# Kernel optimization log

Measured on AMD Instinct MI355X. Metric: run time of the kernel, lower is better.

The kernel has to match this reference:

```python
import jax, jax.numpy as jnp
import numpy as np

NODES = 81
NODE_DIM = 2
IN_DIM = NODES * NODE_DIM  # 162
D = 256
H = 16
HD = D // H
DFF = 2048
T, B, E = 1024, 8, 648


def _layernorm(x, w, b, eps=1e-5):
    m = x.mean(-1, keepdims=True)
    v = x.var(-1, keepdims=True)
    return (x - m) / jnp.sqrt(v + eps) * w + b


def setup_inputs() -> dict:
    key = jax.random.key(0)
    ks = jax.random.split(key, 12)
    s = 0.02
    W = lambda k, shape: jax.random.normal(k, shape, jnp.float32) * s
    return {
        "src": jax.random.normal(ks[0], (T, B, IN_DIM), jnp.float32),
        "edge_index": jax.random.randint(ks[1], (2, E), 0, NODES),
        "gcn_w": W(ks[2], (NODE_DIM, NODE_DIM)),
        "gcn_b": jnp.zeros((NODE_DIM,), jnp.float32),
        "fc_w": W(ks[3], (IN_DIM, D)),
        "fc_b": jnp.zeros((D,), jnp.float32),
        "wq": W(ks[4], (D, D)), "bq": jnp.zeros((D,), jnp.float32),
        "wk": W(ks[5], (D, D)), "bk": jnp.zeros((D,), jnp.float32),
        "wv": W(ks[6], (D, D)), "bv": jnp.zeros((D,), jnp.float32),
        "wo": W(ks[7], (D, D)), "bo": jnp.zeros((D,), jnp.float32),
        "ln1_w": jnp.ones((D,), jnp.float32), "ln1_b": jnp.zeros((D,), jnp.float32),
        "ffn_w1": W(ks[8], (D, DFF)), "ffn_b1": jnp.zeros((DFF,), jnp.float32),
        "ffn_w2": W(ks[9], (DFF, D)), "ffn_b2": jnp.zeros((D,), jnp.float32),
        "ln2_w": jnp.ones((D,), jnp.float32), "ln2_b": jnp.zeros((D,), jnp.float32),
        "dec_w": W(ks[10], (D, IN_DIM)), "dec_b": jnp.zeros((IN_DIM,), jnp.float32),
    }


def reference(src, edge_index, gcn_w, gcn_b, fc_w, fc_b, wq, bq, wk, bk, wv, bv,
              wo, bo, ln1_w, ln1_b, ffn_w1, ffn_b1, ffn_w2, ffn_b2, ln2_w, ln2_b,
              dec_w, dec_b):
    t, b, _ = src.shape
    # ---- batched GCNConv(2,2): all T*B tiny graphs share one adjacency ----
    # src[t,b] = [in_flow(81), out_flow(81)] -> node features [81, 2]
    xg = jnp.swapaxes(src.reshape(t, b, NODE_DIM, NODES), -1, -2)  # [T,B,81,2]
    row, col = edge_index[0], edge_index[1]
    A = jnp.zeros((NODES, NODES), src.dtype).at[col, row].add(1.0)
    A = A + jnp.eye(NODES, dtype=src.dtype)          # add self-loops
    deg = A.sum(1)
    dinv = jnp.where(deg > 0, 1.0 / jnp.sqrt(deg), 0.0)
    A_hat = dinv[:, None] * A * dinv[None, :]        # D^-1/2 (A+I) D^-1/2
    hg = jnp.einsum('ij,tbjc->tbic', A_hat, xg @ gcn_w) + gcn_b  # [T,B,81,2]
    # gcn_output.transpose(0,1).view(-1): channel-major flatten
    src2 = jnp.swapaxes(hg, -1, -2).reshape(t, b, IN_DIM)
    # ---- fc + positional encoding ----
    x = src2 @ fc_w + fc_b  # [T,B,D]
    pos = jnp.arange(t, dtype=jnp.float32)[:, None]
    div = jnp.exp(jnp.arange(0, D, 2, dtype=jnp.float32) * (-np.log(10000.0) / D))
    pe = jnp.zeros((t, D), x.dtype).at[:, 0::2].set(jnp.sin(pos * div))
    pe = pe.at[:, 1::2].set(jnp.cos(pos * div))
    x = x + pe[:, None, :]
    # ---- TransformerEncoderLayer (post-norm, relu, causal mask, eval) ----
    q = (x @ wq + bq).reshape(t, b, H, HD)
    k = (x @ wk + bk).reshape(t, b, H, HD)
    v = (x @ wv + bv).reshape(t, b, H, HD)
    scores = jnp.einsum('tbhd,sbhd->bhts', q, k) / jnp.sqrt(jnp.asarray(HD, x.dtype))
    causal = jnp.tril(jnp.ones((t, t), bool))
    scores = jnp.where(causal, scores, jnp.finfo(x.dtype).min)
    attn = jax.nn.softmax(scores, axis=-1)
    ctx = jnp.einsum('bhts,sbhd->tbhd', attn, v).reshape(t, b, D) @ wo + bo
    x = _layernorm(x + ctx, ln1_w, ln1_b)
    ff = jax.nn.relu(x @ ffn_w1 + ffn_b1) @ ffn_w2 + ffn_b2
    x = _layernorm(x + ff, ln2_w, ln2_b)
    return x @ dec_w + dec_b  # [T,B,162]
```

## Files before the change

### kernel.cpp

```cpp
#include <hip/hip_runtime.h>
#include <math.h>

#define T_    1024
#define B_    8
#define D_    256
#define H_    16
#define HD_   16
#define DFF_  2048
#define NODES_ 81
#define INDIM_ 162
#define E_    648
#define M_    (T_*B_)

typedef __bf16 bf16x8 __attribute__((ext_vector_type(8)));
typedef float  f32x4  __attribute__((ext_vector_type(4)));
typedef unsigned short ushort_t;
typedef unsigned int   uint_t;

union bfpack { bf16x8 v; uint_t u[4]; };

__device__ __forceinline__ ushort_t f2bf(float f) {
    union { float f; uint_t u; } c; c.f = f;
    uint_t u = c.u;
    uint_t r = u + 0x7fffu + ((u >> 16) & 1u);
    return (ushort_t)(r >> 16);
}

__device__ __forceinline__ uint_t fbits(float f) {
    union { float f; uint_t u; } c; c.f = f;
    return c.u;
}

__device__ __forceinline__ float truncbf(float f) {
    union { uint_t u; float f; } c; c.u = fbits(f) & 0xffff0000u;
    return c.f;
}

__device__ __forceinline__ bf16x8 zero8() {
    bf16x8 v;
#pragma unroll
    for (int e = 0; e < 8; e++) v[e] = (__bf16)0.0f;
    return v;
}

__device__ __forceinline__ void gload_lds16(const void* g, void* l) {
    __builtin_amdgcn_global_load_lds(
        (const __attribute__((address_space(1))) void*)g,
        (__attribute__((address_space(3))) void*)l, 16, 0, 0);
}

__device__ __forceinline__ void trans_tile(
        const float* __restrict__ in, ushort_t* __restrict__ out,
        float (*tile)[33], int K, int N, int Kp, int bx, int by) {
    int k0 = bx * 32, n0 = by * 32;
    int tx = threadIdx.x & 31, ty = threadIdx.x >> 5;
#pragma unroll
    for (int i = 0; i < 4; i++) {
        int r = k0 + ty + i * 8, c = n0 + tx;
        tile[ty + i * 8][tx] = (r < K && c < N) ? in[(size_t)r * N + c] : 0.f;
    }
    __syncthreads();
#pragma unroll
    for (int i = 0; i < 4; i++) {
        int r = n0 + ty + i * 8, c = k0 + tx;
        out[(size_t)r * Kp + c] = f2bf(tile[tx][ty + i * 8]);
    }
}

__global__ __launch_bounds__(256) void prep_all(
        const int* __restrict__ edge, const float* __restrict__ gcn_w,
        const float* __restrict__ gcn_b, const float* __restrict__ fc_w,
        const float* __restrict__ fc_b, const float* __restrict__ src,
        const float* __restrict__ wq, const float* __restrict__ wk,
        const float* __restrict__ wv, const float* __restrict__ wo,
        const float* __restrict__ dec_w, const float* __restrict__ w1,
        const float* __restrict__ w2,
        const float* __restrict__ bq, const float* __restrict__ bk,
        const float* __restrict__ bv,
        ushort_t* __restrict__ weffT, float* __restrict__ beff,
        ushort_t* __restrict__ srcb,
        ushort_t* __restrict__ wqkvT, ushort_t* __restrict__ woT,
        ushort_t* __restrict__ dwT, ushort_t* __restrict__ w1T,
        ushort_t* __restrict__ w2T, float* __restrict__ qkvbias) {
    __shared__ float A[NODES_ * NODES_];
    __shared__ float dinv[NODES_];
    __shared__ float tile[32][33];
    int bid = blockIdx.x;
    int tid = threadIdx.x;
    if (bid < 82) {
        for (int i = tid; i < NODES_ * NODES_; i += 256) A[i] = 0.f;
        __syncthreads();
        for (int e = tid; e < E_; e += 256) {
            int r = edge[e];
            int c = edge[E_ + e];
            atomicAdd(&A[c * NODES_ + r], 1.0f);
        }
        __syncthreads();
        if (tid < NODES_) A[tid * NODES_ + tid] += 1.0f;
        __syncthreads();
        if (tid < NODES_) {
            float s = 0.f;
            for (int k = 0; k < NODES_; k++) s += A[tid * NODES_ + k];
            dinv[tid] = (s > 0.f) ? rsqrtf(s) : 0.f;
        }
        __syncthreads();
        int d = tid, j = bid;
        if (j < NODES_) {
            float s0 = 0.f, s1 = 0.f;
            for (int i = 0; i < NODES_; i++) {
                float a = dinv[i] * A[i * NODES_ + j] * dinv[j];
                s0 += a * fc_w[(0 * NODES_ + i) * D_ + d];
                s1 += a * fc_w[(1 * NODES_ + i) * D_ + d];
            }
            weffT[d * 192 + j]          = f2bf(gcn_w[0] * s0 + gcn_w[1] * s1);
            weffT[d * 192 + NODES_ + j] = f2bf(gcn_w[2] * s0 + gcn_w[3] * s1);
        } else {
            float t0 = 0.f, t1 = 0.f;
            for (int i = 0; i < NODES_; i++) {
                t0 += fc_w[(0 * NODES_ + i) * D_ + d];
                t1 += fc_w[(1 * NODES_ + i) * D_ + d];
            }
            beff[d] = fc_b[d] + gcn_b[0] * t0 + gcn_b[1] * t1;
            for (int c = INDIM_; c < 192; c++) weffT[d * 192 + c] = 0;
        }
    } else if (bid < 1426) {
        int l = bid - 82;
        if (l < 64)        trans_tile(wq,    wqkvT,          tile, D_,   D_,     D_,   l & 7,  l >> 3);
        else if (l < 128)  trans_tile(wk,    wqkvT + 65536,  tile, D_,   D_,     D_,   (l-64) & 7,  (l-64) >> 3);
        else if (l < 192)  trans_tile(wv,    wqkvT + 131072, tile, D_,   D_,     D_,   (l-128) & 7, (l-128) >> 3);
        else if (l < 256)  trans_tile(wo,    woT,            tile, D_,   D_,     D_,   (l-192) & 7, (l-192) >> 3);
        else if (l < 320)  trans_tile(dec_w, dwT,            tile, D_,   INDIM_, D_,   (l-256) & 7, (l-256) >> 3);
        else if (l < 832)  trans_tile(w1,    w1T,            tile, D_,   DFF_,   D_,   (l-320) & 7, (l-320) >> 3);
        else               trans_tile(w2,    w2T,            tile, DFF_, D_,     DFF_, (l-832) & 63, (l-832) >> 6);
    } else if (bid == 1426) {
#pragma unroll
        for (int k = 0; k < 3; k++) {
            int i = k * 256 + tid;
            qkvbias[i] = (i < 256) ? bq[i] : ((i < 512) ? bk[i - 256] : bv[i - 512]);
        }
    } else {
        int r = bid - 1427;
        if (tid < 192)
            srcb[(size_t)r * 192 + tid] =
                (tid < INDIM_) ? f2bf(src[(size_t)r * INDIM_ + tid]) : (ushort_t)0;
    }
}

enum { EP_PE = 0, EP_QKV = 1, EP_PLAIN = 2, EP_RELU = 3, EP_DEC = 4, EP_PART = 5 };

template <int EPI, int TM, int KS>
__global__ __launch_bounds__(256) void gemm_bf16(
        const ushort_t* __restrict__ A, const ushort_t* __restrict__ BT,
        const float* __restrict__ bias, float* __restrict__ Cf,
        ushort_t* __restrict__ Cb, int M, int N, int K) {
    __shared__ ushort_t sA[TM * 64];
    __shared__ ushort_t sB[128 * 64];
    int tid = threadIdx.x;
    int w = tid >> 6, lane = tid & 63;
    int cc = lane & 15, q = lane >> 4;
    int bm = blockIdx.y * TM, bn = blockIdx.x * 128;
    int part = (KS > 1) ? blockIdx.z : 0;
    int kbeg = part * (K / KS), kend = kbeg + K / KS;

    int srow = (lane >> 3);
    int sslot = lane & 7;

    const int NJ = (TM == 128) ? 4 : 2;
    int mbase = (TM == 128) ? ((w >> 1) * 64) : 0;
    int nbase = (TM == 128) ? ((w & 1) * 64) : (w * 32);

    f32x4 acc[4][NJ];
#pragma unroll
    for (int i = 0; i < 4; i++)
#pragma unroll
        for (int j = 0; j < NJ; j++)
#pragma unroll
            for (int e = 0; e < 4; e++) acc[i][j][e] = 0.f;

    for (int k0 = kbeg; k0 < kend; k0 += 64) {
        if (TM == 128) {
#pragma unroll
            for (int i = 0; i < 4; i++) {
                int r = w * 32 + i * 8 + srow;
                const ushort_t* ga = A + (size_t)(bm + r) * K + k0 + ((sslot ^ (r & 7)) * 8);
                gload_lds16(ga, &sA[(w * 32 + i * 8) * 64]);
            }
        } else {
#pragma unroll
            for (int i = 0; i < 2; i++) {
                int r = w * 16 + i * 8 + srow;
                const ushort_t* ga = A + (size_t)(bm + r) * K + k0 + ((sslot ^ (r & 7)) * 8);
                gload_lds16(ga, &sA[(w * 16 + i * 8) * 64]);
            }
        }
#pragma unroll
        for (int i = 0; i < 4; i++) {
            int r = w * 32 + i * 8 + srow;
            const ushort_t* gb = BT + (size_t)(bn + r) * K + k0 + ((sslot ^ (r & 7)) * 8);
            gload_lds16(gb, &sB[(w * 32 + i * 8) * 64]);
        }
        __syncthreads();
#pragma unroll
        for (int ks = 0; ks < 2; ks++) {
            bf16x8 af[4], bfr[NJ];
#pragma unroll
            for (int i = 0; i < 4; i++) {
                int m = mbase + i * 16 + cc;
                int off = m * 64 + (((ks * 4 + q) ^ (cc & 7)) * 8);
                af[i] = *(const bf16x8*)&sA[off];
            }
#pragma unroll
            for (int j = 0; j < NJ; j++) {
                int n = nbase + j * 16 + cc;
                int off = n * 64 + (((ks * 4 + q) ^ (cc & 7)) * 8);
                bfr[j] = *(const bf16x8*)&sB[off];
            }
#pragma unroll
            for (int i = 0; i < 4; i++)
#pragma unroll
                for (int j = 0; j < NJ; j++)
                    acc[i][j] = __builtin_amdgcn_mfma_f32_16x16x32_bf16(af[i], bfr[j], acc[i][j], 0, 0, 0);
        }
        __syncthreads();
    }

#pragma unroll
    for (int i = 0; i < 4; i++) {
#pragma unroll
        for (int j = 0; j < NJ; j++) {
            int col = bn + nbase + j * 16 + cc;
            float bv = 0.f;
            if (EPI == EP_DEC) bv = (col < INDIM_) ? bias[col] : 0.f;
            else if (EPI != EP_PART) bv = bias[col];
#pragma unroll
            for (int reg = 0; reg < 4; reg++) {
                int row = bm + mbase + i * 16 + q * 4 + reg;
                float v = acc[i][j][reg] + bv;
                if (EPI == EP_PE) {
                    int t = row >> 3;
                    float freq = __expf((float)(col & ~1) * (-9.210340371976184f / 256.f));
                    float ang = (float)t * freq;
                    v += (col & 1) ? __cosf(ang) : __sinf(ang);
                    Cf[(size_t)row * N + col] = v;
                    Cb[(size_t)row * N + col] = f2bf(v);
                } else if (EPI == EP_QKV) {
                    int t = row >> 3, b = row & 7;
                    int nn = col & 255, which = col >> 8;
                    int h = nn >> 4, hd = nn & 15;
                    Cb[(size_t)which * 2097152 +
                       ((size_t)((b * H_ + h) * T_ + t)) * HD_ + hd] = f2bf(v);
                } else if (EPI == EP_PLAIN) {
                    Cf[(size_t)row * N + col] = v;
                } else if (EPI == EP_RELU) {
                    v = fmaxf(v, 0.f);
                    Cb[(size_t)row * N + col] = f2bf(v);
                } else if (EPI == EP_DEC) {
                    if (col < INDIM_) Cf[(size_t)row * INDIM_ + col] = v;
                } else if (EPI == EP_PART) {
                    Cf[(size_t)part * M * N + (size_t)row * N + col] = v;
                }
            }
        }
    }
}

__global__ __launch_bounds__(256) void attn_mfma(
        const ushort_t* __restrict__ Qb, const ushort_t* __restrict__ Kb,
        const ushort_t* __restrict__ Vb, float* __restrict__ partO,
        float* __restrict__ partL) {
    const int qc_of[20] = {0,1,2,2,3,3,4,4,4,5,5,5,6,6,6,6,7,7,7,7};
    const int kp_of[20] = {0,0,0,1,0,1,0,1,2,0,1,2,0,1,2,3,0,1,2,3};
    int slot = blockIdx.x;
    int qc = qc_of[slot], kp = kp_of[slot];
    int bh = blockIdx.y;
    int tid = threadIdx.x;
    int w = tid >> 6, lane = tid & 63;
    int cc = lane & 15, q = lane >> 4;
    int qb0 = qc * 128;
    int kbeg = kp * 4;
    int kend = 2 * (qc + 1);
    if (kend > kbeg + 4) kend = kbeg + 4;

    __shared__ ushort_t VTs[2][16 * 72];

    const ushort_t* Qp = Qb + (size_t)bh * (T_ * HD_);
    const ushort_t* Kp = Kb + (size_t)bh * (T_ * HD_);
    const ushort_t* Vp = Vb + (size_t)bh * (T_ * HD_);

    bf16x8 qf[2];
#pragma unroll
    for (int i = 0; i < 2; i++) {
        if (q < 2)
            qf[i] = *(const bf16x8*)&Qp[(size_t)(qb0 + w * 32 + i * 16 + cc) * HD_ + q * 8];
        else
            qf[i] = zero8();
    }

    f32x4 ot[2];
    float lacc[2] = {0.f, 0.f};
#pragma unroll
    for (int i = 0; i < 2; i++)
#pragma unroll
        for (int e = 0; e < 4; e++) ot[i][e] = 0.f;

    int qmaxw = qb0 + w * 32 + 31;

    for (int kb = kbeg; kb < kend; kb++) {
        ushort_t* vbuf = VTs[kb & 1];
        if (tid < 128) {
            int r = tid >> 1, half = tid & 1;
            bf16x8 vv = *(const bf16x8*)&Vp[(size_t)(kb * 64 + r) * HD_ + half * 8];
#pragma unroll
            for (int e = 0; e < 8; e++)
                vbuf[(half * 8 + e) * 72 + r] = ((const ushort_t*)&vv)[e];
        }
        __syncthreads();
        if (kb * 64 > qmaxw) continue;

        f32x4 s[2][4];
#pragma unroll
        for (int j = 0; j < 4; j++) {
            bf16x8 kf;
            if (q < 2)
                kf = *(const bf16x8*)&Kp[(size_t)(kb * 64 + j * 16 + cc) * HD_ + q * 8];
            else
                kf = zero8();
#pragma unroll
            for (int i = 0; i < 2; i++) {
                f32x4 z;
#pragma unroll
                for (int e = 0; e < 4; e++) z[e] = 0.f;
                s[i][j] = __builtin_amdgcn_mfma_f32_16x16x32_bf16(kf, qf[i], z, 0, 0, 0);
            }
        }

#pragma unroll
        for (int j = 0; j < 4; j++) {
            bfpack af;
            const uint_t* vt = (const uint_t*)&vbuf[cc * 72 + j * 16 + q * 4];
            af.u[0] = vt[0]; af.u[1] = vt[1]; af.u[2] = 0u; af.u[3] = 0u;
            int key0 = kb * 64 + j * 16 + q * 4;
#pragma unroll
            for (int i = 0; i < 2; i++) {
                int qrow = qb0 + w * 32 + i * 16 + cc;
                float p0 = __expf(s[i][j][0] * 0.25f);
                float p1 = __expf(s[i][j][1] * 0.25f);
                float p2 = __expf(s[i][j][2] * 0.25f);
                float p3 = __expf(s[i][j][3] * 0.25f);
                if (key0 + 0 > qrow) p0 = 0.f;
                if (key0 + 1 > qrow) p1 = 0.f;
                if (key0 + 2 > qrow) p2 = 0.f;
                if (key0 + 3 > qrow) p3 = 0.f;
                bfpack pf;
                pf.u[0] = (fbits(p0) >> 16) | (fbits(p1) & 0xffff0000u);
                pf.u[1] = (fbits(p2) >> 16) | (fbits(p3) & 0xffff0000u);
                pf.u[2] = 0u; pf.u[3] = 0u;
                ot[i] = __builtin_amdgcn_mfma_f32_16x16x32_bf16(af.v, pf.v, ot[i], 0, 0, 0);
                lacc[i] += truncbf(p0) + truncbf(p1) + truncbf(p2) + truncbf(p3);
            }
        }
    }

    int base = (bh * 20 + slot) * 128;
#pragma unroll
    for (int i = 0; i < 2; i++) {
        float l0 = lacc[i];
        l0 += __shfl_xor(l0, 16);
        l0 += __shfl_xor(l0, 32);
        int row = w * 32 + i * 16 + cc;
        *(f32x4*)&partO[((size_t)(base + row)) * 16 + q * 4] = ot[i];
        if (q == 0) partL[base + row] = l0;
    }
}

__global__ __launch_bounds__(256) void attn_reduce(
        const float* __restrict__ partO, const float* __restrict__ partL,
        ushort_t* __restrict__ ctxb) {
    const int cum[9] = {0, 1, 2, 4, 6, 9, 12, 16, 20};
    int qc = blockIdx.x, bh = blockIdx.y;
    int row = threadIdx.x >> 1, dh = threadIdx.x & 1;
    int p0 = cum[qc], p1 = cum[qc + 1];
    float o[8];
#pragma unroll
    for (int e = 0; e < 8; e++) o[e] = 0.f;
    float l = 0.f;
    for (int p = p0; p < p1; p++) {
        size_t base = ((size_t)bh * 20 + p) * 128 + row;
        const float4 a = *(const float4*)&partO[base * 16 + dh * 8];
        const float4 b4 = *(const float4*)&partO[base * 16 + dh * 8 + 4];
        o[0] += a.x; o[1] += a.y; o[2] += a.z; o[3] += a.w;
        o[4] += b4.x; o[5] += b4.y; o[6] += b4.z; o[7] += b4.w;
        l += partL[base];
    }
    float inv = 1.f / l;
    int t = qc * 128 + row, b = bh >> 4, h = bh & 15;
    ushort_t* op = ctxb + ((size_t)t * B_ + b) * D_ + h * HD_ + dh * 8;
    ushort4 u0, u1;
    u0.x = f2bf(o[0] * inv); u0.y = f2bf(o[1] * inv);
    u0.z = f2bf(o[2] * inv); u0.w = f2bf(o[3] * inv);
    u1.x = f2bf(o[4] * inv); u1.y = f2bf(o[5] * inv);
    u1.z = f2bf(o[6] * inv); u1.w = f2bf(o[7] * inv);
    *(ushort4*)&op[0] = u0;
    *(ushort4*)&op[4] = u1;
}

template <int NP, bool HASB>
__global__ __launch_bounds__(256) void ln_kernel(
        const float* __restrict__ X, const float* __restrict__ P0,
        const float* __restrict__ P1, const float* __restrict__ RB,
        const float* __restrict__ w, const float* __restrict__ b,
        float* __restrict__ out, ushort_t* __restrict__ outb) {
    int wv = threadIdx.x >> 6, lane = threadIdx.x & 63;
    int row = blockIdx.x * 4 + wv;
    int c = lane * 4;
    const float4 x4 = *(const float4*)&X[(size_t)row * D_ + c];
    const float4 p4 = *(const float4*)&P0[(size_t)row * D_ + c];
    float v0 = x4.x + p4.x, v1 = x4.y + p4.y, v2 = x4.z + p4.z, v3 = x4.w + p4.w;
    if (NP == 2) {
        const float4 q4 = *(const float4*)&P1[(size_t)row * D_ + c];
        v0 += q4.x; v1 += q4.y; v2 += q4.z; v3 += q4.w;
    }
    if (HASB) {
        const float4 r4 = *(const float4*)&RB[c];
        v0 += r4.x; v1 += r4.y; v2 += r4.z; v3 += r4.w;
    }
    float s  = v0 + v1 + v2 + v3;
    float sq = v0 * v0 + v1 * v1 + v2 * v2 + v3 * v3;
    for (int off = 32; off; off >>= 1) {
        s  += __shfl_xor(s, off);
        sq += __shfl_xor(sq, off);
    }
    float mean = s * (1.f / 256.f);
    float var  = sq * (1.f / 256.f) - mean * mean;
    float rstd = rsqrtf(var + 1e-5f);
    float o0 = (v0 - mean) * rstd * w[c + 0] + b[c + 0];
    float o1 = (v1 - mean) * rstd * w[c + 1] + b[c + 1];
    float o2 = (v2 - mean) * rstd * w[c + 2] + b[c + 2];
    float o3 = (v3 - mean) * rstd * w[c + 3] + b[c + 3];
    float4 o; o.x = o0; o.y = o1; o.z = o2; o.w = o3;
    *(float4*)&out[(size_t)row * D_ + c] = o;
    ushort4 ob;
    ob.x = f2bf(o0); ob.y = f2bf(o1); ob.z = f2bf(o2); ob.w = f2bf(o3);
    *(ushort4*)&outb[(size_t)row * D_ + c] = ob;
}

extern "C" void kernel_launch(void* const* d_in, const int* in_sizes, int n_in,
                              void* d_out, int out_size, void* d_ws, size_t ws_size,
                              hipStream_t stream) {
    (void)in_sizes; (void)n_in; (void)out_size; (void)ws_size;
    const float* src     = (const float*)d_in[0];
    const int*   edge    = (const int*)d_in[1];
    const float* gcn_w   = (const float*)d_in[2];
    const float* gcn_b   = (const float*)d_in[3];
    const float* fc_w    = (const float*)d_in[4];
    const float* fc_b    = (const float*)d_in[5];
    const float* wq      = (const float*)d_in[6];
    const float* bq      = (const float*)d_in[7];
    const float* wk      = (const float*)d_in[8];
    const float* bk      = (const float*)d_in[9];
    const float* wv      = (const float*)d_in[10];
    const float* bv      = (const float*)d_in[11];
    const float* wo      = (const float*)d_in[12];
    const float* bo      = (const float*)d_in[13];
    const float* ln1_w   = (const float*)d_in[14];
    const float* ln1_b   = (const float*)d_in[15];
    const float* ffn_w1  = (const float*)d_in[16];
    const float* ffn_b1  = (const float*)d_in[17];
    const float* ffn_w2  = (const float*)d_in[18];
    const float* ffn_b2  = (const float*)d_in[19];
    const float* ln2_w   = (const float*)d_in[20];
    const float* ln2_b   = (const float*)d_in[21];
    const float* dec_w   = (const float*)d_in[22];
    const float* dec_b   = (const float*)d_in[23];
    float* out = (float*)d_out;

    float* ws = (float*)d_ws;
    float* beff    = ws;
    float* qkvbias = ws + 256;
    float* x0      = ws + 1024;
    float* tmp     = x0  + 2097152;
    float* tmp2    = tmp + 2097152;
    float* x1      = tmp2 + 2097152;
    float* x2s     = x1  + 2097152;
    ushort_t* ub   = (ushort_t*)(ws + 10486784);
    ushort_t* srcb = ub;
    ushort_t* x0b  = ub + 1572864;
    ushort_t* x1b  = x0b + 2097152;
    ushort_t* x2b  = x1b + 2097152;
    ushort_t* ctxb = x2b + 2097152;
    ushort_t* hb   = ctxb + 2097152;
    ushort_t* qkvb = hb + 16777216;
    ushort_t* weffT= qkvb + 6291456;
    ushort_t* wqkvT= weffT + 49152;
    ushort_t* woT  = wqkvT + 196608;
    ushort_t* w1T  = woT + 65536;
    ushort_t* w2T  = w1T + 524288;
    ushort_t* dwT  = w2T + 524288;
    float* partO = (float*)hb;
    float* partL = partO + 5242880;

    prep_all<<<9619, 256, 0, stream>>>(edge, gcn_w, gcn_b, fc_w, fc_b, src,
                                       wq, wk, wv, wo, dec_w, ffn_w1, ffn_w2,
                                       bq, bk, bv, weffT, beff, srcb,
                                       wqkvT, woT, dwT, w1T, w2T, qkvbias);

    gemm_bf16<EP_PE, 64, 1><<<dim3(2, 128), 256, 0, stream>>>(srcb, weffT, beff, x0, x0b, M_, D_, 192);
    gemm_bf16<EP_QKV, 64, 1><<<dim3(6, 128), 256, 0, stream>>>(x0b, wqkvT, qkvbias, nullptr, qkvb, M_, 768, D_);
    attn_mfma<<<dim3(20, 128), 256, 0, stream>>>(qkvb, qkvb + 2097152, qkvb + 4194304, partO, partL);
    attn_reduce<<<dim3(8, 128), 256, 0, stream>>>(partO, partL, ctxb);
    gemm_bf16<EP_PLAIN, 64, 1><<<dim3(2, 128), 256, 0, stream>>>(ctxb, woT, bo, tmp, nullptr, M_, D_, D_);
    ln_kernel<1, false><<<2048, 256, 0, stream>>>(x0, tmp, nullptr, nullptr, ln1_w, ln1_b, x1, x1b);
    gemm_bf16<EP_RELU, 128, 1><<<dim3(16, 64), 256, 0, stream>>>(x1b, w1T, ffn_b1, nullptr, hb, M_, DFF_, D_);
    gemm_bf16<EP_PART, 64, 2><<<dim3(2, 128, 2), 256, 0, stream>>>(hb, w2T, nullptr, tmp, nullptr, M_, D_, DFF_);
    ln_kernel<2, true><<<2048, 256, 0, stream>>>(x1, tmp, tmp2, ffn_b2, ln2_w, ln2_b, x2s, x2b);
    gemm_bf16<EP_DEC, 64, 1><<<dim3(2, 128), 256, 0, stream>>>(x2b, dwT, dec_b, out, nullptr, M_, D_, D_);
}
```

Before: 240.8 us.

## Fuse layernorm into output-projection and FFN2 GEMMs with full-row tiles

Replaces the separate Wo GEMM + LN1 and the split-K FFN2 GEMM + LN2 with a gemm_ln kernel in which each block computes 32 full rows of 256 columns and applies residual add, bias and layernorm in the epilogue. This removes two launches and the fp32 intermediate writes and reads of the partial sums. In exchange, the fused GEMMs run with only 256 blocks, drop the split-K parallelism for the K=2048 GEMM, and reuse each B tile across fewer rows.

```diff
diff --git a/kernel.cpp b/kernel.cpp
--- a/kernel.cpp
+++ b/kernel.cpp
@@ -146,9 +146,9 @@
     }
 }
 
-enum { EP_PE = 0, EP_QKV = 1, EP_PLAIN = 2, EP_RELU = 3, EP_DEC = 4, EP_PART = 5 };
-
-template <int EPI, int TM, int KS>
+enum { EP_PE = 0, EP_QKV = 1, EP_RELU = 3, EP_DEC = 4 };
+
+template <int EPI, int TM>
 __global__ __launch_bounds__(256) void gemm_bf16(
         const ushort_t* __restrict__ A, const ushort_t* __restrict__ BT,
         const float* __restrict__ bias, float* __restrict__ Cf,
@@ -159,8 +159,6 @@
     int w = tid >> 6, lane = tid & 63;
     int cc = lane & 15, q = lane >> 4;
     int bm = blockIdx.y * TM, bn = blockIdx.x * 128;
-    int part = (KS > 1) ? blockIdx.z : 0;
-    int kbeg = part * (K / KS), kend = kbeg + K / KS;
 
     int srow = (lane >> 3);
     int sslot = lane & 7;
@@ -177,7 +175,7 @@
 #pragma unroll
             for (int e = 0; e < 4; e++) acc[i][j][e] = 0.f;
 
-    for (int k0 = kbeg; k0 < kend; k0 += 64) {
+    for (int k0 = 0; k0 < K; k0 += 64) {
         if (TM == 128) {
 #pragma unroll
             for (int i = 0; i < 4; i++) {
@@ -229,9 +227,9 @@
 #pragma unroll
         for (int j = 0; j < NJ; j++) {
             int col = bn + nbase + j * 16 + cc;
-            float bv = 0.f;
+            float bv;
             if (EPI == EP_DEC) bv = (col < INDIM_) ? bias[col] : 0.f;
-            else if (EPI != EP_PART) bv = bias[col];
+            else bv = bias[col];
 #pragma unroll
             for (int reg = 0; reg < 4; reg++) {
                 int row = bm + mbase + i * 16 + q * 4 + reg;
@@ -249,16 +247,135 @@
                     int h = nn >> 4, hd = nn & 15;
                     Cb[(size_t)which * 2097152 +
                        ((size_t)((b * H_ + h) * T_ + t)) * HD_ + hd] = f2bf(v);
-                } else if (EPI == EP_PLAIN) {
-                    Cf[(size_t)row * N + col] = v;
                 } else if (EPI == EP_RELU) {
                     v = fmaxf(v, 0.f);
                     Cb[(size_t)row * N + col] = f2bf(v);
                 } else if (EPI == EP_DEC) {
                     if (col < INDIM_) Cf[(size_t)row * INDIM_ + col] = v;
-                } else if (EPI == EP_PART) {
-                    Cf[(size_t)part * M * N + (size_t)row * N + col] = v;
                 }
+            }
+        }
+    }
+}
+
+template <int K, bool WF>
+__global__ __launch_bounds__(256) void gemm_ln(
+        const ushort_t* __restrict__ A, const ushort_t* __restrict__ BT,
+        const float* __restrict__ bias, const float* __restrict__ X,
+        const float* __restrict__ lnw, const float* __restrict__ lnb,
+        float* __restrict__ Yf, ushort_t* __restrict__ Yb) {
+    __shared__ ushort_t sA[32 * 64];
+    __shared__ ushort_t sB[256 * 64];
+    __shared__ float redS[32 * 4];
+    __shared__ float redQ[32 * 4];
+    int tid = threadIdx.x;
+    int w = tid >> 6, lane = tid & 63;
+    int cc = lane & 15, q = lane >> 4;
+    int bm = blockIdx.x * 32;
+    int srow = lane >> 3, sslot = lane & 7;
+
+    f32x4 acc[2][4];
+#pragma unroll
+    for (int i = 0; i < 2; i++)
+#pragma unroll
+        for (int j = 0; j < 4; j++)
+#pragma unroll
+            for (int e = 0; e < 4; e++) acc[i][j][e] = 0.f;
+
+    for (int k0 = 0; k0 < K; k0 += 64) {
+        {
+            int r = w * 8 + srow;
+            const ushort_t* ga = A + (size_t)(bm + r) * K + k0 + ((sslot ^ (r & 7)) * 8);
+            gload_lds16(ga, &sA[(w * 8) * 64]);
+        }
+#pragma unroll
+        for (int i = 0; i < 8; i++) {
+            int r = i * 32 + w * 8 + srow;
+            const ushort_t* gb = BT + (size_t)r * K + k0 + ((sslot ^ (r & 7)) * 8);
+            gload_lds16(gb, &sB[(i * 32 + w * 8) * 64]);
+        }
+        __syncthreads();
+#pragma unroll
+        for (int ks = 0; ks < 2; ks++) {
+            bf16x8 af[2], bfr[4];
+#pragma unroll
+            for (int i = 0; i < 2; i++) {
+                int m = i * 16 + cc;
+                af[i] = *(const bf16x8*)&sA[m * 64 + (((ks * 4 + q) ^ (cc & 7)) * 8)];
+            }
+#pragma unroll
+            for (int j = 0; j < 4; j++) {
+                int n = w * 64 + j * 16 + cc;
+                bfr[j] = *(const bf16x8*)&sB[n * 64 + (((ks * 4 + q) ^ (cc & 7)) * 8)];
+            }
+#pragma unroll
+            for (int i = 0; i < 2; i++)
+#pragma unroll
+                for (int j = 0; j < 4; j++)
+                    acc[i][j] = __builtin_amdgcn_mfma_f32_16x16x32_bf16(af[i], bfr[j], acc[i][j], 0, 0, 0);
+        }
+        __syncthreads();
+    }
+
+    float ls[2][4], lq[2][4];
+#pragma unroll
+    for (int i = 0; i < 2; i++)
+#pragma unroll
+        for (int reg = 0; reg < 4; reg++) { ls[i][reg] = 0.f; lq[i][reg] = 0.f; }
+#pragma unroll
+    for (int i = 0; i < 2; i++) {
+#pragma unroll
+        for (int j = 0; j < 4; j++) {
+            int col = w * 64 + j * 16 + cc;
+            float bv = bias[col];
+#pragma unroll
+            for (int reg = 0; reg < 4; reg++) {
+                int row = bm + i * 16 + q * 4 + reg;
+                float t = acc[i][j][reg] + bv + X[(size_t)row * D_ + col];
+                acc[i][j][reg] = t;
+                ls[i][reg] += t;
+                lq[i][reg] += t * t;
+            }
+        }
+    }
+#pragma unroll
+    for (int m = 1; m < 16; m <<= 1) {
+#pragma unroll
+        for (int i = 0; i < 2; i++)
+#pragma unroll
+            for (int reg = 0; reg < 4; reg++) {
+                ls[i][reg] += __shfl_xor(ls[i][reg], m);
+                lq[i][reg] += __shfl_xor(lq[i][reg], m);
+            }
+    }
+    if (cc == 0) {
+#pragma unroll
+        for (int i = 0; i < 2; i++)
+#pragma unroll
+            for (int reg = 0; reg < 4; reg++) {
+                int r = i * 16 + q * 4 + reg;
+                redS[r * 4 + w] = ls[i][reg];
+                redQ[r * 4 + w] = lq[i][reg];
+            }
+    }
+    __syncthreads();
+#pragma unroll
+    for (int i = 0; i < 2; i++) {
+#pragma unroll
+        for (int reg = 0; reg < 4; reg++) {
+            int r = i * 16 + q * 4 + reg;
+            float S  = redS[r * 4 + 0] + redS[r * 4 + 1] + redS[r * 4 + 2] + redS[r * 4 + 3];
+            float Q2 = redQ[r * 4 + 0] + redQ[r * 4 + 1] + redQ[r * 4 + 2] + redQ[r * 4 + 3];
+            float mean = S * (1.f / 256.f);
+            float var  = Q2 * (1.f / 256.f) - mean * mean;
+            float rstd = rsqrtf(var + 1e-5f);
+            int row = bm + r;
+#pragma unroll
+            for (int j = 0; j < 4; j++) {
+                int col = w * 64 + j * 16 + cc;
+                float y = (acc[i][j][reg] - mean) * rstd * lnw[col] + lnb[col];
+                if (WF) Yf[(size_t)row * D_ + col] = y;
+                Yb[(size_t)row * D_ + col] = f2bf(y);
             }
         }
     }
@@ -402,46 +519,6 @@
     u1.z = f2bf(o[6] * inv); u1.w = f2bf(o[7] * inv);
     *(ushort4*)&op[0] = u0;
     *(ushort4*)&op[4] = u1;
-}
-
-template <int NP, bool HASB>
-__global__ __launch_bounds__(256) void ln_kernel(
-        const float* __restrict__ X, const float* __restrict__ P0,
-        const float* __restrict__ P1, const float* __restrict__ RB,
-        const float* __restrict__ w, const float* __restrict__ b,
-        float* __restrict__ out, ushort_t* __restrict__ outb) {
-    int wv = threadIdx.x >> 6, lane = threadIdx.x & 63;
-    int row = blockIdx.x * 4 + wv;
-    int c = lane * 4;
-    const float4 x4 = *(const float4*)&X[(size_t)row * D_ + c];
-    const float4 p4 = *(const float4*)&P0[(size_t)row * D_ + c];
-    float v0 = x4.x + p4.x, v1 = x4.y + p4.y, v2 = x4.z + p4.z, v3 = x4.w + p4.w;
-    if (NP == 2) {
-        const float4 q4 = *(const float4*)&P1[(size_t)row * D_ + c];
-        v0 += q4.x; v1 += q4.y; v2 += q4.z; v3 += q4.w;
-    }
-    if (HASB) {
-        const float4 r4 = *(const float4*)&RB[c];
-        v0 += r4.x; v1 += r4.y; v2 += r4.z; v3 += r4.w;
-    }
-    float s  = v0 + v1 + v2 + v3;
-    float sq = v0 * v0 + v1 * v1 + v2 * v2 + v3 * v3;
-    for (int off = 32; off; off >>= 1) {
-        s  += __shfl_xor(s, off);
-        sq += __shfl_xor(sq, off);
-    }
-    float mean = s * (1.f / 256.f);
-    float var  = sq * (1.f / 256.f) - mean * mean;
-    float rstd = rsqrtf(var + 1e-5f);
-    float o0 = (v0 - mean) * rstd * w[c + 0] + b[c + 0];
-    float o1 = (v1 - mean) * rstd * w[c + 1] + b[c + 1];
-    float o2 = (v2 - mean) * rstd * w[c + 2] + b[c + 2];
-    float o3 = (v3 - mean) * rstd * w[c + 3] + b[c + 3];
-    float4 o; o.x = o0; o.y = o1; o.z = o2; o.w = o3;
-    *(float4*)&out[(size_t)row * D_ + c] = o;
-    ushort4 ob;
-    ob.x = f2bf(o0); ob.y = f2bf(o1); ob.z = f2bf(o2); ob.w = f2bf(o3);
-    *(ushort4*)&outb[(size_t)row * D_ + c] = ob;
 }
 
 extern "C" void kernel_launch(void* const* d_in, const int* in_sizes, int n_in,
@@ -478,11 +555,8 @@
     float* beff    = ws;
     float* qkvbias = ws + 256;
     float* x0      = ws + 1024;
-    float* tmp     = x0  + 2097152;
-    float* tmp2    = tmp + 2097152;
-    float* x1      = tmp2 + 2097152;
-    float* x2s     = x1  + 2097152;
-    ushort_t* ub   = (ushort_t*)(ws + 10486784);
+    float* x1      = x0 + 2097152;
+    ushort_t* ub   = (ushort_t*)(ws + 4195328);
     ushort_t* srcb = ub;
     ushort_t* x0b  = ub + 1572864;
     ushort_t* x1b  = x0b + 2097152;
@@ -504,14 +578,12 @@
                                        bq, bk, bv, weffT, beff, srcb,
                                        wqkvT, woT, dwT, w1T, w2T, qkvbias);
 
-    gemm_bf16<EP_PE, 64, 1><<<dim3(2, 128), 256, 0, stream>>>(srcb, weffT, beff, x0, x0b, M_, D_, 192);
-    gemm_bf16<EP_QKV, 64, 1><<<dim3(6, 128), 256, 0, stream>>>(x0b, wqkvT, qkvbias, nullptr, qkvb, M_, 768, D_);
+    gemm_bf16<EP_PE, 64><<<dim3(2, 128), 256, 0, stream>>>(srcb, weffT, beff, x0, x0b, M_, D_, 192);
+    gemm_bf16<EP_QKV, 64><<<dim3(6, 128), 256, 0, stream>>>(x0b, wqkvT, qkvbias, nullptr, qkvb, M_, 768, D_);
     attn_mfma<<<dim3(20, 128), 256, 0, stream>>>(qkvb, qkvb + 2097152, qkvb + 4194304, partO, partL);
     attn_reduce<<<dim3(8, 128), 256, 0, stream>>>(partO, partL, ctxb);
-    gemm_bf16<EP_PLAIN, 64, 1><<<dim3(2, 128), 256, 0, stream>>>(ctxb, woT, bo, tmp, nullptr, M_, D_, D_);
-    ln_kernel<1, false><<<2048, 256, 0, stream>>>(x0, tmp, nullptr, nullptr, ln1_w, ln1_b, x1, x1b);
-    gemm_bf16<EP_RELU, 128, 1><<<dim3(16, 64), 256, 0, stream>>>(x1b, w1T, ffn_b1, nullptr, hb, M_, DFF_, D_);
-    gemm_bf16<EP_PART, 64, 2><<<dim3(2, 128, 2), 256, 0, stream>>>(hb, w2T, nullptr, tmp, nullptr, M_, D_, DFF_);
-    ln_kernel<2, true><<<2048, 256, 0, stream>>>(x1, tmp, tmp2, ffn_b2, ln2_w, ln2_b, x2s, x2b);
-    gemm_bf16<EP_DEC, 64, 1><<<dim3(2, 128), 256, 0, stream>>>(x2b, dwT, dec_b, out, nullptr, M_, D_, D_);
-}
+    gemm_ln<256, true><<<256, 256, 0, stream>>>(ctxb, woT, bo, x0, ln1_w, ln1_b, x1, x1b);
+    gemm_bf16<EP_RELU, 128><<<dim3(16, 64), 256, 0, stream>>>(x1b, w1T, ffn_b1, nullptr, hb, M_, DFF_, D_);
+    gemm_ln<2048, false><<<256, 256, 0, stream>>>(hb, w2T, ffn_b2, x1, ln2_w, ln2_b, nullptr, x2b);
+    gemm_bf16<EP_DEC, 64><<<dim3(2, 128), 256, 0, stream>>>(x2b, dwT, dec_b, out, nullptr, M_, D_, D_);
+}
```

After: 246.0 us. 2.1% more time.

## Fold softmax scale into Q, compute row sums via MFMA, skip unneeded causal masks

Applied to the files above, without the earlier changes.

The 1/sqrt(HD) scale moves into the QKV epilogue, so Q is stored pre-scaled and the per-score multiply before exp disappears. The softmax denominator is now accumulated with an extra MFMA against a ones vector instead of scalar truncation adds plus cross-lane shuffles. Causal masking is applied only to tiles that straddle the diagonal. V transpose loading is spread over all 256 threads, and the K fragments are hoisted ahead of the score MFMAs. The extra MFMA per tile adds matrix-core work, and rounding Q to bf16 after scaling slightly changes numerics.

```diff
diff --git a/kernel.cpp b/kernel.cpp
--- a/kernel.cpp
+++ b/kernel.cpp
@@ -29,11 +29,6 @@
 __device__ __forceinline__ uint_t fbits(float f) {
     union { float f; uint_t u; } c; c.f = f;
     return c.u;
-}
-
-__device__ __forceinline__ float truncbf(float f) {
-    union { uint_t u; float f; } c; c.u = fbits(f) & 0xffff0000u;
-    return c.f;
 }
 
 __device__ __forceinline__ bf16x8 zero8() {
@@ -247,8 +242,9 @@
                     int t = row >> 3, b = row & 7;
                     int nn = col & 255, which = col >> 8;
                     int h = nn >> 4, hd = nn & 15;
+                    float vq = (which == 0) ? v * 0.25f : v;
                     Cb[(size_t)which * 2097152 +
-                       ((size_t)((b * H_ + h) * T_ + t)) * HD_ + hd] = f2bf(v);
+                       ((size_t)((b * H_ + h) * T_ + t)) * HD_ + hd] = f2bf(vq);
                 } else if (EPI == EP_PLAIN) {
                     Cf[(size_t)row * N + col] = v;
                 } else if (EPI == EP_RELU) {
@@ -296,43 +292,50 @@
             qf[i] = zero8();
     }
 
-    f32x4 ot[2];
-    float lacc[2] = {0.f, 0.f};
+    bf16x8 ones8;
+#pragma unroll
+    for (int e = 0; e < 8; e++) ones8[e] = (__bf16)1.0f;
+
+    f32x4 ot[2], ls[2];
 #pragma unroll
     for (int i = 0; i < 2; i++)
 #pragma unroll
-        for (int e = 0; e < 4; e++) ot[i][e] = 0.f;
+        for (int e = 0; e < 4; e++) { ot[i][e] = 0.f; ls[i][e] = 0.f; }
 
     int qmaxw = qb0 + w * 32 + 31;
 
     for (int kb = kbeg; kb < kend; kb++) {
         ushort_t* vbuf = VTs[kb & 1];
-        if (tid < 128) {
-            int r = tid >> 1, half = tid & 1;
-            bf16x8 vv = *(const bf16x8*)&Vp[(size_t)(kb * 64 + r) * HD_ + half * 8];
-#pragma unroll
-            for (int e = 0; e < 8; e++)
-                vbuf[(half * 8 + e) * 72 + r] = ((const ushort_t*)&vv)[e];
+        {
+            int r = tid >> 2, c0 = (tid & 3) * 4;
+            ushort4 vv = *(const ushort4*)&Vp[(size_t)(kb * 64 + r) * HD_ + c0];
+            vbuf[(c0 + 0) * 72 + r] = vv.x;
+            vbuf[(c0 + 1) * 72 + r] = vv.y;
+            vbuf[(c0 + 2) * 72 + r] = vv.z;
+            vbuf[(c0 + 3) * 72 + r] = vv.w;
         }
         __syncthreads();
         if (kb * 64 > qmaxw) continue;
 
+        bf16x8 kf[4];
+#pragma unroll
+        for (int j = 0; j < 4; j++) {
+            if (q < 2)
+                kf[j] = *(const bf16x8*)&Kp[(size_t)(kb * 64 + j * 16 + cc) * HD_ + q * 8];
+            else
+                kf[j] = zero8();
+        }
+
         f32x4 s[2][4];
 #pragma unroll
-        for (int j = 0; j < 4; j++) {
-            bf16x8 kf;
-            if (q < 2)
-                kf = *(const bf16x8*)&Kp[(size_t)(kb * 64 + j * 16 + cc) * HD_ + q * 8];
-            else
-                kf = zero8();
+        for (int j = 0; j < 4; j++)
 #pragma unroll
             for (int i = 0; i < 2; i++) {
                 f32x4 z;
 #pragma unroll
                 for (int e = 0; e < 4; e++) z[e] = 0.f;
-                s[i][j] = __builtin_amdgcn_mfma_f32_16x16x32_bf16(kf, qf[i], z, 0, 0, 0);
-            }
-        }
+                s[i][j] = __builtin_amdgcn_mfma_f32_16x16x32_bf16(kf[j], qf[i], z, 0, 0, 0);
+            }
 
 #pragma unroll
         for (int j = 0; j < 4; j++) {
@@ -342,21 +345,23 @@
             int key0 = kb * 64 + j * 16 + q * 4;
 #pragma unroll
             for (int i = 0; i < 2; i++) {
-                int qrow = qb0 + w * 32 + i * 16 + cc;
-                float p0 = __expf(s[i][j][0] * 0.25f);
-                float p1 = __expf(s[i][j][1] * 0.25f);
-                float p2 = __expf(s[i][j][2] * 0.25f);
-                float p3 = __expf(s[i][j][3] * 0.25f);
-                if (key0 + 0 > qrow) p0 = 0.f;
-                if (key0 + 1 > qrow) p1 = 0.f;
-                if (key0 + 2 > qrow) p2 = 0.f;
-                if (key0 + 3 > qrow) p3 = 0.f;
+                float p0 = __expf(s[i][j][0]);
+                float p1 = __expf(s[i][j][1]);
+                float p2 = __expf(s[i][j][2]);
+                float p3 = __expf(s[i][j][3]);
+                if (kb * 64 + j * 16 + 15 > qb0 + w * 32 + i * 16) {
+                    int qrow = qb0 + w * 32 + i * 16 + cc;
+                    if (key0 + 0 > qrow) p0 = 0.f;
+                    if (key0 + 1 > qrow) p1 = 0.f;
+                    if (key0 + 2 > qrow) p2 = 0.f;
+                    if (key0 + 3 > qrow) p3 = 0.f;
+                }
                 bfpack pf;
                 pf.u[0] = (fbits(p0) >> 16) | (fbits(p1) & 0xffff0000u);
                 pf.u[1] = (fbits(p2) >> 16) | (fbits(p3) & 0xffff0000u);
                 pf.u[2] = 0u; pf.u[3] = 0u;
                 ot[i] = __builtin_amdgcn_mfma_f32_16x16x32_bf16(af.v, pf.v, ot[i], 0, 0, 0);
-                lacc[i] += truncbf(p0) + truncbf(p1) + truncbf(p2) + truncbf(p3);
+                ls[i] = __builtin_amdgcn_mfma_f32_16x16x32_bf16(ones8, pf.v, ls[i], 0, 0, 0);
             }
         }
     }
@@ -364,12 +369,9 @@
     int base = (bh * 20 + slot) * 128;
 #pragma unroll
     for (int i = 0; i < 2; i++) {
-        float l0 = lacc[i];
-        l0 += __shfl_xor(l0, 16);
-        l0 += __shfl_xor(l0, 32);
         int row = w * 32 + i * 16 + cc;
         *(f32x4*)&partO[((size_t)(base + row)) * 16 + q * 4] = ot[i];
-        if (q == 0) partL[base + row] = l0;
+        if (q == 0) partL[base + row] = ls[i][0];
     }
 }
 
```

Measured after the change: 234.8 us. 2.5% less time.
